# Kernel tuning notes

Hardware: AMD Instinct MI355X
Metric: run time of the kernel (lower is better)

## Reference

```python
import jax, jax.numpy as jnp
import numpy as np

B, T, C, H = 2, 2048, 1024, 16
Dh = C // H  # 64
EPS = 1e-5


def layer_norm(x, g, b):
    mu = jnp.mean(x, axis=-1, keepdims=True)
    var = jnp.mean(jnp.square(x - mu), axis=-1, keepdims=True)
    return (x - mu) * jax.lax.rsqrt(var + EPS) * g + b


def setup_inputs() -> dict:
    key = jax.random.key(0)
    ks = jax.random.split(key, 12)
    s = 0.02
    return {
        "x": jax.random.normal(ks[0], (B, T, C), dtype=jnp.float32),
        # per-head projections, stacked: (H, C, Dh), no bias (bias=False in source)
        "Wq": jax.random.normal(ks[1], (H, C, Dh), dtype=jnp.float32) * s,
        "Wk": jax.random.normal(ks[2], (H, C, Dh), dtype=jnp.float32) * s,
        "Wv": jax.random.normal(ks[3], (H, C, Dh), dtype=jnp.float32) * s,
        "Wo": jax.random.normal(ks[4], (H * Dh, C), dtype=jnp.float32) * s,
        "bo": jnp.zeros((C,), dtype=jnp.float32),
        "W1": jax.random.normal(ks[5], (C, 4 * C), dtype=jnp.float32) * s,
        "b1": jnp.zeros((4 * C,), dtype=jnp.float32),
        "W2": jax.random.normal(ks[6], (4 * C, C), dtype=jnp.float32) * s,
        "b2": jnp.zeros((C,), dtype=jnp.float32),
        "g1": jnp.ones((C,), dtype=jnp.float32),
        "be1": jnp.zeros((C,), dtype=jnp.float32),
        "g2": jnp.ones((C,), dtype=jnp.float32),
        "be2": jnp.zeros((C,), dtype=jnp.float32),
    }


def reference(x, Wq, Wk, Wv, Wo, bo, W1, b1, W2, b2, g1, be1, g2, be2):
    # --- self-attention sublayer ---
    h = layer_norm(x, g1, be1)                       # (B,T,C)
    q = jnp.einsum("btc,hcd->bhtd", h, Wq)
    k = jnp.einsum("btc,hcd->bhtd", h, Wk)
    v = jnp.einsum("btc,hcd->bhtd", h, Wv)
    # NOTE: source scales by C**-0.5 (head INPUT dim), not head_size**-0.5
    scores = jnp.einsum("bhqd,bhkd->bhqk", q, k) * (C ** -0.5)
    # encoder=True default => mask is all ones => no masking applied
    w = jax.nn.softmax(scores, axis=-1)              # (B,H,T,T)
    o = jnp.einsum("bhqk,bhkd->bhqd", w, v)          # (B,H,T,Dh)
    o = o.transpose(0, 2, 1, 3).reshape(B, T, H * Dh)  # concat heads
    attn = o @ Wo + bo                               # output projection
    x = x + attn
    # --- feed-forward sublayer ---
    h2 = layer_norm(x, g2, be2)
    ff = jax.nn.relu(h2 @ W1 + b1) @ W2 + b2
    return x + ff
```

## Files before the change

### kernel.cpp

```cpp
#include <hip/hip_runtime.h>
#include <hip/hip_bf16.h>

#define BT   4096
#define CD   1024
#define TD   2048
#define NH   16
#define DH   64
#define BB   2

typedef __attribute__((ext_vector_type(8))) short bf16x8;
typedef __attribute__((ext_vector_type(4))) short bf16x4;
typedef __attribute__((ext_vector_type(4))) float f32x4;
typedef __attribute__((ext_vector_type(2))) unsigned int u32x2;
typedef __attribute__((ext_vector_type(4))) unsigned int u32x4;

__device__ inline short f2bf(float f) {
    union { float fv; unsigned u; } x; x.fv = f;
    unsigned r = x.u + 0x7fffu + ((x.u >> 16) & 1u);
    return (short)(r >> 16);
}
__device__ inline float bf2f(short s) {
    union { unsigned u; float f; } x; x.u = ((unsigned)(unsigned short)s) << 16;
    return x.f;
}
__device__ inline unsigned pk2bf(float a, float b) {
    union { __hip_bfloat162 h; unsigned u; } cv;
    cv.h = __float22bfloat162_rn(float2{a, b});
    return cv.u;
}

#if __has_builtin(__builtin_amdgcn_exp2f)
#define EXP2(x) __builtin_amdgcn_exp2f(x)
#else
#define EXP2(x) exp2f(x)
#endif

__device__ inline void gload_lds16(const short* g, short* lds) {
    __builtin_amdgcn_global_load_lds(
        (const __attribute__((address_space(1))) void*)g,
        (__attribute__((address_space(3))) void*)lds, 16, 0, 0);
}

__launch_bounds__(256)
__global__ void ln_kernel(const float* __restrict__ x,
                          const float* __restrict__ g,
                          const float* __restrict__ be,
                          short* __restrict__ out) {
    __shared__ float red[2][4];
    const int row = blockIdx.x;
    const int c4 = threadIdx.x * 4;
    const float* xr = x + (size_t)row * CD;
    float4 v = *(const float4*)&xr[c4];
    float s  = (v.x + v.y) + (v.z + v.w);
    float ss = (v.x * v.x + v.y * v.y) + (v.z * v.z + v.w * v.w);
    #pragma unroll
    for (int off = 32; off > 0; off >>= 1) {
        s  += __shfl_down(s,  off, 64);
        ss += __shfl_down(ss, off, 64);
    }
    int wid = threadIdx.x >> 6, lane = threadIdx.x & 63;
    if (lane == 0) { red[0][wid] = s; red[1][wid] = ss; }
    __syncthreads();
    float sum   = red[0][0] + red[0][1] + red[0][2] + red[0][3];
    float sumsq = red[1][0] + red[1][1] + red[1][2] + red[1][3];
    float mu   = sum * (1.f / CD);
    float var  = sumsq * (1.f / CD) - mu * mu;
    float rstd = rsqrtf(var + 1e-5f);
    float4 gv = *(const float4*)&g[c4];
    float4 bv = *(const float4*)&be[c4];
    bf16x4 o;
    o[0] = f2bf((v.x - mu) * rstd * gv.x + bv.x);
    o[1] = f2bf((v.y - mu) * rstd * gv.y + bv.y);
    o[2] = f2bf((v.z - mu) * rstd * gv.z + bv.z);
    o[3] = f2bf((v.w - mu) * rstd * gv.w + bv.w);
    *(bf16x4*)&out[(size_t)row * CD + c4] = o;
}

__launch_bounds__(256)
__global__ void prep_weights(const float* __restrict__ Wq, const float* __restrict__ Wk,
                             const float* __restrict__ Wv, const float* __restrict__ Wo,
                             const float* __restrict__ W1, const float* __restrict__ W2,
                             short* __restrict__ wqt, short* __restrict__ wot,
                             short* __restrict__ w1t, short* __restrict__ w2t) {
    __shared__ float tt[64][65];
    const int id = blockIdx.x;
    const float* in; short* out; int R, Cc, r0, c0;
    if (id < 768) {
        int which = id >> 8, rem = id & 255, hh = rem >> 4, ry = rem & 15;
        in  = (which == 0 ? Wq : which == 1 ? Wk : Wv) + (size_t)hh * CD * DH;
        out = wqt + (size_t)which * CD * CD + (size_t)hh * DH * CD;
        R = CD; Cc = DH; r0 = ry * 64; c0 = 0;
    } else if (id < 1024) {
        int t = id - 768;  in = Wo; out = wot; R = CD;     Cc = CD;     r0 = (t >> 4) * 64; c0 = (t & 15) * 64;
    } else if (id < 2048) {
        int t = id - 1024; in = W1; out = w1t; R = CD;     Cc = 4 * CD; r0 = (t >> 6) * 64; c0 = (t & 63) * 64;
    } else {
        int t = id - 2048; in = W2; out = w2t; R = 4 * CD; Cc = CD;     r0 = (t >> 4) * 64; c0 = (t & 15) * 64;
    }
    const int tid = threadIdx.x;
    #pragma unroll
    for (int i = 0; i < 4; ++i) {
        int f = i * 256 + tid;
        int r = f >> 4, cc = (f & 15) * 4;
        float4 vv = *(const float4*)&in[(size_t)(r0 + r) * Cc + c0 + cc];
        tt[r][cc]     = vv.x;
        tt[r][cc + 1] = vv.y;
        tt[r][cc + 2] = vv.z;
        tt[r][cc + 3] = vv.w;
    }
    __syncthreads();
    #pragma unroll
    for (int i = 0; i < 16; ++i) {
        int e = i * 256 + tid;
        out[(size_t)(c0 + (e >> 6)) * R + r0 + (e & 63)] = f2bf(tt[e & 63][e >> 6]);
    }
}

__launch_bounds__(256)
__global__ void vtrans(const short* __restrict__ vin, short* __restrict__ vout) {
    __shared__ short t[64 * 65];
    const int tid = threadIdx.x;
    const int bh = blockIdx.y;
    const int t0 = blockIdx.x * 64;
    const int b = bh >> 4, h = bh & 15;
    const short* src = vin + (size_t)b * TD * CD + (size_t)h * DH;
    short* dst = vout + (size_t)bh * DH * TD;
    #pragma unroll
    for (int i = 0; i < 16; ++i) {
        int e = i * 256 + tid;
        t[(e >> 6) * 65 + (e & 63)] = src[(size_t)(t0 + (e >> 6)) * CD + (e & 63)];
    }
    __syncthreads();
    #pragma unroll
    for (int i = 0; i < 16; ++i) {
        int e = i * 256 + tid;
        int d = e >> 6, tt = e & 63;
        dst[(size_t)d * TD + t0 + tt] = t[tt * 65 + d];
    }
}

template <int MODE, int TN, int GR>
__launch_bounds__(GR * 256)
__global__ void gemm_mfma(const short* __restrict__ A,
                          const short* __restrict__ Bt,
                          const float* __restrict__ bias,
                          const float* __restrict__ resid,
                          float* __restrict__ outf,
                          short* __restrict__ outb,
                          int N, int K) {
    __shared__ __align__(16) short smem[GR * 3 * (128 + TN) * 32];
    const int tid = threadIdx.x;
    const int kgrp = (GR == 2) ? (tid >> 8) : 0;
    const int tid256 = tid & 255;
    const int w4 = tid256 >> 6, lane = tid & 63;
    const int quad = lane >> 4, l16 = lane & 15;
    const int wr = w4 >> 1, wc = w4 & 1;
    const int li = blockIdx.y * gridDim.x + blockIdx.x;
    const int m0 = ((li & 7) * 4 + ((li >> 3) & 3)) * 128;
    const int n0 = (li >> 5) * TN;
    const int NT = TN / 32;
    const int kbase = kgrp * (K / GR);

    short* grpBase = smem + (size_t)kgrp * 3 * (128 + TN) * 32;
#define AS(bi) (grpBase + (bi) * (128 + TN) * 32)
#define BS(bi) (AS(bi) + 128 * 32)

    f32x4 acc[4][NT] = {};

    auto STAGE = [&](int kt, int bi) {
        const int k0 = kbase + kt * 32;
        short* as = AS(bi);
        short* bs = BS(bi);
        #pragma unroll
        for (int i = 0; i < 2; ++i) {
            int s = i * 256 + tid256;
            int row = s >> 2, kc = (s & 3) ^ ((row >> 1) & 3);
            gload_lds16(A + (size_t)(m0 + row) * K + k0 + kc * 8,
                        &as[(i * 256 + w4 * 64) * 8]);
        }
        #pragma unroll
        for (int i = 0; i < TN / 64; ++i) {
            int s = i * 256 + tid256;
            int row = s >> 2, kc = (s & 3) ^ ((row >> 1) & 3);
            gload_lds16(Bt + (size_t)(n0 + row) * K + k0 + kc * 8,
                        &bs[(i * 256 + w4 * 64) * 8]);
        }
    };

    auto COMPUTE = [&](int bi) {
        const int xo = (quad ^ ((l16 >> 1) & 3)) * 8;
        const short* as = AS(bi);
        const short* bs = BS(bi);
        bf16x8 a[4], b[NT];
        #pragma unroll
        for (int mt = 0; mt < 4; ++mt)
            a[mt] = *(const bf16x8*)&as[(wr * 64 + mt * 16 + l16) * 32 + xo];
        #pragma unroll
        for (int nt = 0; nt < NT; ++nt)
            b[nt] = *(const bf16x8*)&bs[(wc * (TN / 2) + nt * 16 + l16) * 32 + xo];
        #pragma unroll
        for (int mt = 0; mt < 4; ++mt)
            #pragma unroll
            for (int nt = 0; nt < NT; ++nt)
                acc[mt][nt] = __builtin_amdgcn_mfma_f32_16x16x32_bf16(a[mt], b[nt], acc[mt][nt], 0, 0, 0);
    };

    const int nk = (K / GR) >> 5;
    STAGE(0, 0);
    STAGE(1, 1);
    int bi = 0;
    for (int t = 0; t < nk - 1; ++t) {
        if (TN == 256) asm volatile("s_waitcnt vmcnt(6)" ::: "memory");
        else           asm volatile("s_waitcnt vmcnt(4)" ::: "memory");
        __builtin_amdgcn_s_barrier();
        asm volatile("" ::: "memory");
        int bn = bi + 2 >= 3 ? bi - 1 : bi + 2;
        if (t + 2 < nk) STAGE(t + 2, bn);
        COMPUTE(bi);
        bi = bi + 1 >= 3 ? 0 : bi + 1;
    }
    asm volatile("s_waitcnt vmcnt(0)" ::: "memory");
    __builtin_amdgcn_s_barrier();
    asm volatile("" ::: "memory");
    COMPUTE(bi);

    if (GR == 2) {
        float* red = (float*)smem;
        __syncthreads();
        if (kgrp == 1) {
            #pragma unroll
            for (int mt = 0; mt < 4; ++mt)
                #pragma unroll
                for (int nt = 0; nt < NT; ++nt)
                    *(f32x4*)&red[((mt * NT + nt) * 256 + w4 * 64 + lane) * 4] = acc[mt][nt];
        }
        __syncthreads();
        if (kgrp == 1) return;
        #pragma unroll
        for (int mt = 0; mt < 4; ++mt)
            #pragma unroll
            for (int nt = 0; nt < NT; ++nt) {
                f32x4 p = *(const f32x4*)&red[((mt * NT + nt) * 256 + w4 * 64 + lane) * 4];
                acc[mt][nt] += p;
            }
    }

    const float qsc = (MODE == 5 && n0 < CD) ? 0.03125f * 1.44269504f : 1.0f;
    short* ob5 = (MODE == 5) ? outb + (size_t)(n0 >> 10) * BT * CD : nullptr;

    #pragma unroll
    for (int mt = 0; mt < 4; ++mt)
        #pragma unroll
        for (int nt = 0; nt < NT; ++nt)
            #pragma unroll
            for (int reg = 0; reg < 4; ++reg) {
                int row = m0 + wr * 64 + mt * 16 + quad * 4 + reg;
                int col = n0 + wc * (TN / 2) + nt * 16 + l16;
                float v = acc[mt][nt][reg];
                if (MODE == 1) { v += bias[col] + resid[(size_t)row * N + col];
                                 outf[(size_t)row * N + col] = v; }
                if (MODE == 2) { v = fmaxf(v + bias[col], 0.f);
                                 outb[(size_t)row * N + col] = f2bf(v); }
                if (MODE == 5) { ob5[(size_t)row * CD + (col & 1023)] = f2bf(v * qsc); }
            }
#undef AS
#undef BS
}

#define BQ   128
#define BK   32

__launch_bounds__(256, 5)
__global__ void attn_mfma(const short* __restrict__ q,
                          const short* __restrict__ k,
                          const short* __restrict__ vt,
                          short* __restrict__ opart,
                          float* __restrict__ lpart) {
    __shared__ short Ks[3][BK * DH];
    __shared__ short Vt[3][DH * BK];

    const int tid  = threadIdx.x;
    const int w = tid >> 6, lane = tid & 63;
    const int quad = lane >> 4, l16 = lane & 15;
    const int h = blockIdx.y;
    const int b = blockIdx.z >> 1, split = blockIdx.z & 1;
    const int q0 = blockIdx.x * BQ;
    const size_t base  = (size_t)b * TD * CD + (size_t)h * DH;
    const size_t vbase = (size_t)(b * NH + h) * DH * TD;

    bf16x8 qf[2][2];
    #pragma unroll
    for (int rt = 0; rt < 2; ++rt) {
        const short* qp = q + base + (size_t)(q0 + w * 32 + rt * 16 + l16) * CD;
        qf[rt][0] = *(const bf16x8*)&qp[quad * 8];
        qf[rt][1] = *(const bf16x8*)&qp[32 + quad * 8];
    }

    const bf16x8 ones = {(short)0x3F80, (short)0x3F80, (short)0x3F80, (short)0x3F80,
                         (short)0x3F80, (short)0x3F80, (short)0x3F80, (short)0x3F80};
    f32x4 O_l[2] = {};
    f32x4 O[2][4] = {};

    const int kbeg = split * (TD / 2);
    const int NTI = (TD / 2) / BK;

    const int ks  = tid >> 3;
    const int kc  = (tid & 7) ^ (ks & 7);
    const int kkey = (((ks & 15) >> 2) << 3) + (ks & 3) + ((ks >> 4) << 2);
    const short* kgp = k + base + (size_t)kkey * CD + kc * 8;
    const int vd = tid >> 2;
    const int vc = (tid & 3) ^ ((vd >> 1) & 3);
    const short* vgp = vt + vbase + (size_t)vd * TD + vc * 8;

#define STAGE_T(kt, bi) do {                                              \
        const size_t ko_ = (size_t)(kbeg + (kt) * BK);                    \
        gload_lds16(kgp + ko_ * CD, &Ks[bi][w * 512]);                    \
        gload_lds16(vgp + ko_,      &Vt[bi][w * 512]);                    \
    } while (0)

#define COMPUTE_T(bi) do {                                                \
        __builtin_amdgcn_s_setprio(1);                                    \
        const int kswz = l16 & 7;                                         \
        bf16x8 kbe0 = *(const bf16x8*)&Ks[bi][l16 * 64 + ((quad) ^ kswz) * 8];        \
        bf16x8 kbe1 = *(const bf16x8*)&Ks[bi][l16 * 64 + ((4 + quad) ^ kswz) * 8];    \
        bf16x8 kbo0 = *(const bf16x8*)&Ks[bi][(16 + l16) * 64 + ((quad) ^ kswz) * 8]; \
        bf16x8 kbo1 = *(const bf16x8*)&Ks[bi][(16 + l16) * 64 + ((4 + quad) ^ kswz) * 8]; \
        bf16x8 pa8[2];                                                    \
        _Pragma("unroll")                                                 \
        for (int rt = 0; rt < 2; ++rt) {                                  \
            f32x4 ae = (f32x4){0.f, 0.f, 0.f, 0.f};                       \
            f32x4 ao = (f32x4){0.f, 0.f, 0.f, 0.f};                       \
            ae = __builtin_amdgcn_mfma_f32_16x16x32_bf16(kbe0, qf[rt][0], ae, 0, 0, 0); \
            ae = __builtin_amdgcn_mfma_f32_16x16x32_bf16(kbe1, qf[rt][1], ae, 0, 0, 0); \
            ao = __builtin_amdgcn_mfma_f32_16x16x32_bf16(kbo0, qf[rt][0], ao, 0, 0, 0); \
            ao = __builtin_amdgcn_mfma_f32_16x16x32_bf16(kbo1, qf[rt][1], ao, 0, 0, 0); \
            float pe0 = EXP2(ae[0]), pe1 = EXP2(ae[1]);                   \
            float pe2 = EXP2(ae[2]), pe3 = EXP2(ae[3]);                   \
            float po0 = EXP2(ao[0]), po1 = EXP2(ao[1]);                   \
            float po2 = EXP2(ao[2]), po3 = EXP2(ao[3]);                   \
            union { u32x4 u; bf16x8 s; } cv_;                             \
            cv_.u = (u32x4){pk2bf(pe0, pe1), pk2bf(pe2, pe3),             \
                            pk2bf(po0, po1), pk2bf(po2, po3)};            \
            pa8[rt] = cv_.s;                                              \
        }                                                                 \
        const int vswz = (l16 >> 1) & 3;                                  \
        _Pragma("unroll")                                                 \
        for (int dt = 0; dt < 4; ++dt) {                                  \
            bf16x8 vb = *(const bf16x8*)&Vt[bi][(dt * 16 + l16) * 32 + ((quad) ^ vswz) * 8]; \
            O[0][dt] = __builtin_amdgcn_mfma_f32_16x16x32_bf16(pa8[0], vb, O[0][dt], 0, 0, 0); \
            O[1][dt] = __builtin_amdgcn_mfma_f32_16x16x32_bf16(pa8[1], vb, O[1][dt], 0, 0, 0); \
        }                                                                 \
        O_l[0] = __builtin_amdgcn_mfma_f32_16x16x32_bf16(pa8[0], ones, O_l[0], 0, 0, 0); \
        O_l[1] = __builtin_amdgcn_mfma_f32_16x16x32_bf16(pa8[1], ones, O_l[1], 0, 0, 0); \
        __builtin_amdgcn_s_setprio(0);                                    \
    } while (0)

    STAGE_T(0, 0);
    STAGE_T(1, 1);
    int bi = 0;
    for (int t = 0; t < NTI - 1; ++t) {
        asm volatile("s_waitcnt vmcnt(2)" ::: "memory");
        __builtin_amdgcn_s_barrier();
        asm volatile("" ::: "memory");
        int bn = bi + 2 >= 3 ? bi - 1 : bi + 2;
        if (t + 2 < NTI) STAGE_T(t + 2, bn);
        COMPUTE_T(bi);
        bi = bi + 1 >= 3 ? 0 : bi + 1;
    }
    asm volatile("s_waitcnt vmcnt(0)" ::: "memory");
    __builtin_amdgcn_s_barrier();
    asm volatile("" ::: "memory");
    COMPUTE_T(bi);
#undef STAGE_T
#undef COMPUTE_T

    short* osp = opart + (size_t)split * BT * CD;
    float* lsp = lpart + (size_t)split * BB * NH * TD + (size_t)(b * NH + h) * TD;
    #pragma unroll
    for (int rt = 0; rt < 2; ++rt) {
        if (l16 == 0)
            *(f32x4*)&lsp[q0 + w * 32 + rt * 16 + quad * 4] = O_l[rt];
        #pragma unroll
        for (int reg = 0; reg < 4; ++reg) {
            int row = q0 + w * 32 + rt * 16 + quad * 4 + reg;
            short* op = osp + base + (size_t)row * CD;
            #pragma unroll
            for (int dt = 0; dt < 4; ++dt)
                op[dt * 16 + l16] = f2bf(O[rt][dt][reg]);
        }
    }
}

__launch_bounds__(256)
__global__ void attn_combine(const short* __restrict__ opart,
                             const float* __restrict__ lpart,
                             short* __restrict__ ob) {
    const size_t idx = ((size_t)blockIdx.x * 256 + threadIdx.x) * 8;
    const int row = (int)(idx >> 10);
    const int col = (int)(idx & 1023);
    const int b = row >> 11, qq = row & (TD - 1), hh = col >> 6;
    const size_t lbase = (size_t)(b * NH + hh) * TD + qq;
    const float l0 = lpart[lbase];
    const float l1 = lpart[(size_t)BB * NH * TD + lbase];
    const float inv = 1.f / (l0 + l1);
    bf16x8 a = *(const bf16x8*)&opart[idx];
    bf16x8 c = *(const bf16x8*)&opart[(size_t)BT * CD + idx];
    bf16x8 r;
    #pragma unroll
    for (int j = 0; j < 8; ++j)
        r[j] = f2bf((bf2f(a[j]) + bf2f(c[j])) * inv);
    *(bf16x8*)&ob[idx] = r;
}

extern "C" void kernel_launch(void* const* d_in, const int* in_sizes, int n_in,
                              void* d_out, int out_size, void* d_ws, size_t ws_size,
                              hipStream_t stream) {
    const float* x   = (const float*)d_in[0];
    const float* Wq  = (const float*)d_in[1];
    const float* Wk  = (const float*)d_in[2];
    const float* Wv  = (const float*)d_in[3];
    const float* Wo  = (const float*)d_in[4];
    const float* bo  = (const float*)d_in[5];
    const float* W1  = (const float*)d_in[6];
    const float* b1  = (const float*)d_in[7];
    const float* W2  = (const float*)d_in[8];
    const float* b2  = (const float*)d_in[9];
    const float* g1  = (const float*)d_in[10];
    const float* be1 = (const float*)d_in[11];
    const float* g2  = (const float*)d_in[12];
    const float* be2 = (const float*)d_in[13];
    float* out = (float*)d_out;

    const size_t SZ = (size_t)BT * CD;
    float* ws  = (float*)d_ws;
    short* qbf = (short*)ws;
    short* kbf = qbf + SZ;
    short* vbf = qbf + 2 * SZ;
    float* lpart = ws + SZ + SZ / 2;
    short* opart = (short*)(ws + 2 * SZ);
    float* x1  = ws + 2 * SZ;
    short* h   = (short*)(ws + 3 * SZ);
    short* ob  = (short*)(ws + 3 * SZ + SZ / 2);
    short* wqt = (short*)(ws + 4 * SZ);
    short* wot = wqt + 3 * CD * CD;
    short* w1t = (short*)(ws + 4 * SZ + SZ / 2);
    short* w2t = (short*)(ws + 5 * SZ);
    short* vtg = (short*)(ws + 5 * SZ + SZ / 2);
    short* ff1 = (short*)ws;

    ln_kernel<<<BT, 256, 0, stream>>>(x, g1, be1, h);

    prep_weights<<<3072, 256, 0, stream>>>(Wq, Wk, Wv, Wo, W1, W2, wqt, wot, w1t, w2t);

    gemm_mfma<5, 128, 1><<<dim3(24, 32), 256, 0, stream>>>(h, wqt, nullptr, nullptr, nullptr, qbf, 3 * CD, CD);

    vtrans<<<dim3(TD / 64, 2 * NH), 256, 0, stream>>>(vbf, vtg);

    attn_mfma<<<dim3(TD / BQ, NH, BB * 2), 256, 0, stream>>>(qbf, kbf, vtg, opart, lpart);

    attn_combine<<<dim3((int)(SZ / (256 * 8))), 256, 0, stream>>>(opart, lpart, ob);

    gemm_mfma<1, 128, 2><<<dim3(8, 32), 512, 0, stream>>>(ob, wot, bo, x, x1, nullptr, CD, CD);

    ln_kernel<<<BT, 256, 0, stream>>>(x1, g2, be2, h);

    gemm_mfma<2, 256, 1><<<dim3(16, 32), 256, 0, stream>>>(h, w1t, b1, nullptr, nullptr, ff1, 4 * CD, CD);

    gemm_mfma<1, 128, 2><<<dim3(8, 32), 512, 0, stream>>>(ff1, w2t, b2, x1, out, nullptr, CD, 4 * CD);
}
```

Measured before the change: 317.3 us.

## Restructure attention K/V pipeline into four-buffer ring with paired tile compute

The attention kernel's LDS ring for K and V^T tiles grows from three to four buffers, and the main loop now computes two key tiles per iteration. Both are then refilled together after a second barrier, so there are fewer waitcnt/barrier pairs per tile and the loads run further ahead of compute. Priority raising now brackets the pair of computes instead of each one. In exchange, LDS use per block rises, the occupancy hint drops from 5 to 4 blocks, and the extra barrier before refilling can stall waves.

```diff
diff --git a/kernel.cpp b/kernel.cpp
--- a/kernel.cpp
+++ b/kernel.cpp
@@ -270,14 +270,14 @@
 #define BQ   128
 #define BK   32
 
-__launch_bounds__(256, 5)
+__launch_bounds__(256, 4)
 __global__ void attn_mfma(const short* __restrict__ q,
                           const short* __restrict__ k,
                           const short* __restrict__ vt,
                           short* __restrict__ opart,
                           float* __restrict__ lpart) {
-    __shared__ short Ks[3][BK * DH];
-    __shared__ short Vt[3][DH * BK];
+    __shared__ short Ks[4][BK * DH];
+    __shared__ short Vt[4][DH * BK];
 
     const int tid  = threadIdx.x;
     const int w = tid >> 6, lane = tid & 63;
@@ -319,7 +319,6 @@
     } while (0)
 
 #define COMPUTE_T(bi) do {                                                \
-        __builtin_amdgcn_s_setprio(1);                                    \
         const int kswz = l16 & 7;                                         \
         bf16x8 kbe0 = *(const bf16x8*)&Ks[bi][l16 * 64 + ((quad) ^ kswz) * 8];        \
         bf16x8 kbe1 = *(const bf16x8*)&Ks[bi][l16 * 64 + ((4 + quad) ^ kswz) * 8];    \
@@ -352,25 +351,38 @@
         }                                                                 \
         O_l[0] = __builtin_amdgcn_mfma_f32_16x16x32_bf16(pa8[0], ones, O_l[0], 0, 0, 0); \
         O_l[1] = __builtin_amdgcn_mfma_f32_16x16x32_bf16(pa8[1], ones, O_l[1], 0, 0, 0); \
-        __builtin_amdgcn_s_setprio(0);                                    \
     } while (0)
 
     STAGE_T(0, 0);
     STAGE_T(1, 1);
-    int bi = 0;
-    for (int t = 0; t < NTI - 1; ++t) {
-        asm volatile("s_waitcnt vmcnt(2)" ::: "memory");
+    STAGE_T(2, 2);
+    STAGE_T(3, 3);
+    for (int it = 0; it < NTI - 2; it += 2) {
+        const int b0 = it & 3;
+        asm volatile("s_waitcnt vmcnt(4)" ::: "memory");
         __builtin_amdgcn_s_barrier();
         asm volatile("" ::: "memory");
-        int bn = bi + 2 >= 3 ? bi - 1 : bi + 2;
-        if (t + 2 < NTI) STAGE_T(t + 2, bn);
-        COMPUTE_T(bi);
-        bi = bi + 1 >= 3 ? 0 : bi + 1;
+        __builtin_amdgcn_s_setprio(1);
+        COMPUTE_T(b0);
+        COMPUTE_T(b0 + 1);
+        __builtin_amdgcn_s_setprio(0);
+        __builtin_amdgcn_s_barrier();
+        asm volatile("" ::: "memory");
+        if (it + 4 < NTI) {
+            STAGE_T(it + 4, b0);
+            STAGE_T(it + 5, b0 + 1);
+        }
     }
     asm volatile("s_waitcnt vmcnt(0)" ::: "memory");
     __builtin_amdgcn_s_barrier();
     asm volatile("" ::: "memory");
-    COMPUTE_T(bi);
+    {
+        const int b0 = (NTI - 2) & 3;
+        __builtin_amdgcn_s_setprio(1);
+        COMPUTE_T(b0);
+        COMPUTE_T(b0 + 1);
+        __builtin_amdgcn_s_setprio(0);
+    }
 #undef STAGE_T
 #undef COMPUTE_T
 
```

After: 320.8 us. About the same (+1.1%).
